# Kernel optimization log

Hardware: AMD Instinct MI355X
Metric: run time of the kernel (lower is better)

The kernel has to match this reference:

```python
import jax, jax.numpy as jnp
import numpy as np

D_MODEL = 1024
D_STATE = 16
D_CONV = 4
EXPAND = 2
D_INNER = EXPAND * D_MODEL          # 2048
DT_RANK = (D_MODEL + 15) // 16      # 64
B_SZ, L = 2, 2048


def setup_inputs() -> dict:
    key = jax.random.key(0)
    ks = jax.random.split(key, 14)
    s = 0.02
    dt_init = jax.random.uniform(ks[10], (D_INNER,), minval=1e-3, maxval=0.1)
    A = jnp.tile(jnp.arange(1, D_STATE + 1, dtype=jnp.float32)[None, :], (D_INNER, 1))
    return {
        "x_f": jax.random.normal(ks[0], (B_SZ, L, D_MODEL), jnp.float32),
        "x_h": jax.random.normal(ks[1], (B_SZ, L, D_MODEL), jnp.float32),
        "W_hf": s * jax.random.normal(ks[2], (D_MODEL, D_MODEL), jnp.float32),
        "b_hf": jnp.zeros((D_MODEL,), jnp.float32),
        "W_in": s * jax.random.normal(ks[3], (2 * D_INNER, D_MODEL), jnp.float32),
        "conv_w": s * jax.random.normal(ks[4], (D_INNER, 1, D_CONV), jnp.float32),
        "conv_b": jnp.zeros((D_INNER,), jnp.float32),
        "W_x": s * jax.random.normal(ks[5], (DT_RANK + 2 * D_STATE, D_INNER), jnp.float32),
        "W_dt": (DT_RANK ** -0.5) * jax.random.normal(ks[6], (D_INNER, DT_RANK), jnp.float32),
        "b_dt": jnp.log(jnp.expm1(dt_init)),
        "A_log": jnp.log(A),
        "D": jnp.ones((D_INNER,), jnp.float32),
        "W_out": s * jax.random.normal(ks[7], (D_MODEL, D_INNER), jnp.float32),
    }


def _mamba(x, W_in, conv_w, conv_b, W_x, W_dt, b_dt, A_log, D, W_out):
    B, Lx, _ = x.shape
    # in_proj -> x, z branches  [B, L, 2*d_inner]
    xz = jnp.einsum("bld,ed->ble", x, W_in)
    x_in, z = jnp.split(xz, 2, axis=-1)
    # causal depthwise conv1d, kernel d_conv, groups = d_inner
    x_nch = jnp.transpose(x_in, (0, 2, 1))  # [B, d_inner, L]
    x_conv = jax.lax.conv_general_dilated(
        x_nch, conv_w, window_strides=(1,), padding=[(D_CONV - 1, 0)],
        dimension_numbers=("NCH", "OIH", "NCH"), feature_group_count=D_INNER)
    x_c = jax.nn.silu(jnp.transpose(x_conv, (0, 2, 1)) + conv_b)  # [B, L, d_inner]
    # input-dependent dt, B, C
    x_dbl = jnp.einsum("ble,fe->blf", x_c, W_x)
    dt_r = x_dbl[..., :DT_RANK]
    B_ssm = x_dbl[..., DT_RANK:DT_RANK + D_STATE]          # [B, L, d_state]
    C_ssm = x_dbl[..., DT_RANK + D_STATE:]                  # [B, L, d_state]
    dt = jax.nn.softplus(jnp.einsum("blr,er->ble", dt_r, W_dt) + b_dt)  # [B, L, d_inner]
    A = -jnp.exp(A_log)  # [d_inner, d_state]

    # selective scan over time; carry h: [B, d_inner, d_state]
    def step(h, inp):
        dt_t, B_t, C_t, x_t = inp  # [B,d_inner], [B,d_state], [B,d_state], [B,d_inner]
        dA = jnp.exp(dt_t[:, :, None] * A)                       # [B, d_inner, d_state]
        dBx = dt_t[:, :, None] * B_t[:, None, :] * x_t[:, :, None]
        h = dA * h + dBx
        y_t = jnp.einsum("bes,bs->be", h, C_t)
        return h, y_t

    seq = (jnp.transpose(dt, (1, 0, 2)), jnp.transpose(B_ssm, (1, 0, 2)),
           jnp.transpose(C_ssm, (1, 0, 2)), jnp.transpose(x_c, (1, 0, 2)))
    h0 = jnp.zeros((B, D_INNER, D_STATE), x.dtype)
    _, ys = jax.lax.scan(step, h0, seq)
    y = jnp.transpose(ys, (1, 0, 2)) + D * x_c   # skip term
    y = y * jax.nn.silu(z)                        # output gate
    return jnp.einsum("ble,de->bld", y, W_out)


def reference(x_f, x_h, W_hf, b_hf, W_in, conv_w, conv_b, W_x, W_dt, b_dt, A_log, D, W_out):
    hf_gate = jax.nn.sigmoid(jnp.einsum("bld,ed->ble", x_h, W_hf) + b_hf)
    modulated = x_f * hf_gate
    return _mamba(modulated, W_in, conv_w, conv_b, W_x, W_dt, b_dt, A_log, D, W_out)
```

## Files before the change

kernel.cpp:

```cpp
#include <hip/hip_runtime.h>
#include <hip/hip_bf16.h>
#include <math.h>

#define L_SEQ  2048
#define BATCH  2
#define DMODEL 1024
#define DINNER 2048
#define DSTATE 16
#define NCHUNK 32
#define LCH    (L_SEQ / NCHUNK)

typedef __attribute__((ext_vector_type(8))) short bf16x8;
typedef __attribute__((ext_vector_type(4))) float f32x4;

__device__ __forceinline__ unsigned short f2bu(float x) {
    __hip_bfloat16 h = __float2bfloat16(x);
    return __builtin_bit_cast(unsigned short, h);
}
__device__ __forceinline__ float fast_exp2(float x) {
    float r; asm("v_exp_f32 %0, %1" : "=v"(r) : "v"(x)); return r;
}
#define LOG2E 1.44269504088896f

__global__ __launch_bounds__(256) void cvt_bf16(
    const float* __restrict__ s, __hip_bfloat16* __restrict__ d)
{
    const int i = (blockIdx.x * 256 + threadIdx.x) * 4;
    const float4 v = *reinterpret_cast<const float4*>(&s[i]);
    ushort4 u;
    u.x = f2bu(v.x); u.y = f2bu(v.y); u.z = f2bu(v.z); u.w = f2bu(v.w);
    *reinterpret_cast<ushort4*>(&d[i]) = u;
}

__global__ __launch_bounds__(256) void cvt_pad_wx(
    const float* __restrict__ s, __hip_bfloat16* __restrict__ d)
{
    const int i = (blockIdx.x * 256 + threadIdx.x) * 4;
    const int r = i >> 11;
    ushort4 u = {0, 0, 0, 0};
    if (r < 96) {
        const float4 v = *reinterpret_cast<const float4*>(&s[i]);
        u.x = f2bu(v.x); u.y = f2bu(v.y); u.z = f2bu(v.z); u.w = f2bu(v.w);
    }
    *reinterpret_cast<ushort4*>(&d[i]) = u;
}

template <int EPI>
__global__ __launch_bounds__(256) void mfma_gemm(
    const __hip_bfloat16* __restrict__ A, int lda,
    const __hip_bfloat16* __restrict__ Bw, int ldb,
    int ksz,
    float* __restrict__ Cf, int ldc,
    __hip_bfloat16* __restrict__ Cb,
    __hip_bfloat16* __restrict__ Cb2,
    const float* __restrict__ bias,
    const float* __restrict__ mul, int ldmul)
{
    __shared__ unsigned short As[2][128 * 32];
    __shared__ unsigned short Bs[2][128 * 32];
    const int tid = threadIdx.x;
    const int row0 = blockIdx.y * 128;
    const int col0 = blockIdx.x * 128;
    const int wid = tid >> 6, lane = tid & 63;
    const int wr = wid >> 1, wc = wid & 1;
    const int fr = lane & 15, fq = lane >> 4;
    const int kz0 = blockIdx.z * ksz;

    f32x4 acc[4][4];
#pragma unroll
    for (int i = 0; i < 4; i++)
#pragma unroll
        for (int j = 0; j < 4; j++) acc[i][j] = (f32x4){0.f, 0.f, 0.f, 0.f};

    const int i0 = tid, i1 = tid + 256;
    const size_t ga0 = (size_t)(row0 + (i0 >> 2)) * lda + (i0 & 3) * 8;
    const size_t ga1 = (size_t)(row0 + (i1 >> 2)) * lda + (i1 & 3) * 8;
    const size_t gb0 = (size_t)(col0 + (i0 >> 2)) * ldb + (i0 & 3) * 8;
    const size_t gb1 = (size_t)(col0 + (i1 >> 2)) * ldb + (i1 & 3) * 8;
    const int nk = ksz >> 5;

#if __has_builtin(__builtin_amdgcn_global_load_lds)
    auto STAGE = [&](int buf, int koff) {
        __builtin_amdgcn_global_load_lds(
            (const __attribute__((address_space(1))) unsigned int*)(A + ga0 + koff),
            (__attribute__((address_space(3))) unsigned int*)&As[buf][i0 * 8], 16, 0, 0);
        __builtin_amdgcn_global_load_lds(
            (const __attribute__((address_space(1))) unsigned int*)(A + ga1 + koff),
            (__attribute__((address_space(3))) unsigned int*)&As[buf][i1 * 8], 16, 0, 0);
        __builtin_amdgcn_global_load_lds(
            (const __attribute__((address_space(1))) unsigned int*)(Bw + gb0 + koff),
            (__attribute__((address_space(3))) unsigned int*)&Bs[buf][i0 * 8], 16, 0, 0);
        __builtin_amdgcn_global_load_lds(
            (const __attribute__((address_space(1))) unsigned int*)(Bw + gb1 + koff),
            (__attribute__((address_space(3))) unsigned int*)&Bs[buf][i1 * 8], 16, 0, 0);
    };
    STAGE(0, kz0);
    __syncthreads();
    for (int kk = 0; kk < nk; kk++) {
        const int cur = kk & 1;
        if (kk + 1 < nk) STAGE(cur ^ 1, kz0 + (kk + 1) * 32);
        bf16x8 af[4], bq[4];
#pragma unroll
        for (int rb = 0; rb < 4; rb++)
            af[rb] = *reinterpret_cast<const bf16x8*>(
                &As[cur][(wr * 64 + rb * 16 + fr) * 32 + fq * 8]);
#pragma unroll
        for (int cb = 0; cb < 4; cb++)
            bq[cb] = *reinterpret_cast<const bf16x8*>(
                &Bs[cur][(wc * 64 + cb * 16 + fr) * 32 + fq * 8]);
#pragma unroll
        for (int rb = 0; rb < 4; rb++)
#pragma unroll
            for (int cb = 0; cb < 4; cb++)
                acc[rb][cb] = __builtin_amdgcn_mfma_f32_16x16x32_bf16(
                    af[rb], bq[cb], acc[rb][cb], 0, 0, 0);
        __syncthreads();
    }
#else
    for (int kk = 0; kk < nk; kk++) {
        const int koff = kz0 + kk * 32;
        const uint4 va0 = *reinterpret_cast<const uint4*>(A + ga0 + koff);
        const uint4 va1 = *reinterpret_cast<const uint4*>(A + ga1 + koff);
        const uint4 vb0 = *reinterpret_cast<const uint4*>(Bw + gb0 + koff);
        const uint4 vb1 = *reinterpret_cast<const uint4*>(Bw + gb1 + koff);
        __syncthreads();
        *reinterpret_cast<uint4*>(&As[0][i0 * 8]) = va0;
        *reinterpret_cast<uint4*>(&As[0][i1 * 8]) = va1;
        *reinterpret_cast<uint4*>(&Bs[0][i0 * 8]) = vb0;
        *reinterpret_cast<uint4*>(&Bs[0][i1 * 8]) = vb1;
        __syncthreads();
        bf16x8 af[4], bq[4];
#pragma unroll
        for (int rb = 0; rb < 4; rb++)
            af[rb] = *reinterpret_cast<const bf16x8*>(
                &As[0][(wr * 64 + rb * 16 + fr) * 32 + fq * 8]);
#pragma unroll
        for (int cb = 0; cb < 4; cb++)
            bq[cb] = *reinterpret_cast<const bf16x8*>(
                &Bs[0][(wc * 64 + cb * 16 + fr) * 32 + fq * 8]);
#pragma unroll
        for (int rb = 0; rb < 4; rb++)
#pragma unroll
            for (int cb = 0; cb < 4; cb++)
                acc[rb][cb] = __builtin_amdgcn_mfma_f32_16x16x32_bf16(
                    af[rb], bq[cb], acc[rb][cb], 0, 0, 0);
    }
#endif

    float* Cz = Cf;
    if (EPI == 0)
        Cz = Cf + (size_t)blockIdx.z * (size_t)(gridDim.y * 128) * ldc;
    const int r0 = row0 + wr * 64, c0 = col0 + wc * 64;
#pragma unroll
    for (int rb = 0; rb < 4; rb++)
#pragma unroll
        for (int cb = 0; cb < 4; cb++) {
            const int col = c0 + cb * 16 + fr;
#pragma unroll
            for (int j = 0; j < 4; j++) {
                const int row = r0 + rb * 16 + fq * 4 + j;
                float v = acc[rb][cb][j];
                if (EPI == 0) {
                    Cz[(size_t)row * ldc + col] = v;
                } else if (EPI == 1) {
                    v = 1.f / (1.f + __expf(-(v + bias[col])));
                    v *= mul[(size_t)row * ldmul + col];
                    Cb[(size_t)row * ldc + col] = __float2bfloat16(v);
                } else if (EPI == 2) {
                    if (col0 < 2048) Cb[(size_t)row * 2048 + col] = __float2bfloat16(v);
                    else             Cb2[(size_t)row * 2048 + col - 2048] = __float2bfloat16(v);
                } else {
                    v += bias[col];
                    v = (v > 20.f) ? v : log1pf(__expf(v));
                    Cf[(size_t)row * ldc + col] = v;
                }
            }
        }
}

__global__ __launch_bounds__(256) void reduce_xdbl(
    const float* __restrict__ part, float* __restrict__ xdbl,
    __hip_bfloat16* __restrict__ dtr)
{
    const int i = blockIdx.x * 256 + threadIdx.x;
    float s = 0.f;
#pragma unroll
    for (int j = 0; j < 4; j++) s += part[(size_t)j * 524288 + i];
    xdbl[i] = s;
    const int col = i & 127;
    if (col < 64) dtr[((i >> 7) << 6) + col] = __float2bfloat16(s);
}

__global__ __launch_bounds__(256) void conv_silu_kernel(
    const __hip_bfloat16* __restrict__ xin_b, const float* __restrict__ cw,
    const float* __restrict__ cb, __hip_bfloat16* __restrict__ xcb)
{
    int gid = blockIdx.x * 256 + threadIdx.x;
    int e = gid & (DINNER - 1);
    int row = gid >> 11;
    int t = row & (L_SEQ - 1);
    float s = cb[e];
#pragma unroll
    for (int j = 0; j < 4; j++) {
        int tt = t - 3 + j;
        if (tt >= 0)
            s = fmaf(cw[e * 4 + j],
                     __bfloat162float(xin_b[(size_t)(row - 3 + j) * 2048 + e]), s);
    }
    xcb[(size_t)row * 2048 + e] = __float2bfloat16(s / (1.f + __expf(-s)));
}

__global__ __launch_bounds__(256) void scan_pass_a(
    const float* __restrict__ dtp, const __hip_bfloat16* __restrict__ xcb,
    const float* __restrict__ xdbl, const float* __restrict__ A_log,
    float* __restrict__ hloc, float* __restrict__ Pp)
{
    __shared__ float sB[LCH][16];
    const int tid = threadIdx.x;
    const int e = (blockIdx.x << 8) + tid;
    const int chunk = blockIdx.y;
    const int b = blockIdx.z;
    const int t0 = chunk * LCH;

    {
        const int r = tid >> 2, sl = tid & 3;
        *(float4*)&sB[r][sl * 4] =
            *(const float4*)&xdbl[(size_t)(b * L_SEQ + t0 + r) * 128 + 64 + sl * 4];
    }
    float av[16];
#pragma unroll
    for (int sq = 0; sq < 4; sq++) {
        const float4 al = *(const float4*)&A_log[e * 16 + sq * 4];
#pragma unroll
        for (int j = 0; j < 4; j++)
            av[sq * 4 + j] = -fast_exp2(((const float*)&al)[j] * LOG2E);
    }
    float h[16];
#pragma unroll
    for (int s = 0; s < 16; s++) h[s] = 0.f;
    float sdt = 0.f;
    __syncthreads();

    const size_t rb = (size_t)(b * L_SEQ + t0) * 2048 + e;
    float dtv_n = dtp[rb];
    float xv_n = __bfloat162float(xcb[rb]);
    for (int t = 0; t < LCH; t++) {
        const float dtv = dtv_n, xv = xv_n;
        if (t + 1 < LCH) {
            dtv_n = dtp[rb + (size_t)(t + 1) * 2048];
            xv_n = __bfloat162float(xcb[rb + (size_t)(t + 1) * 2048]);
        }
        sdt += dtv;
        const float dtx = dtv * xv;
        const float dl2 = dtv * LOG2E;
#pragma unroll
        for (int sq = 0; sq < 4; sq++) {
            const float4 B4 = *(const float4*)&sB[t][sq * 4];
#pragma unroll
            for (int j = 0; j < 4; j++) {
                const int s = sq * 4 + j;
                const float Bv = ((const float*)&B4)[j];
                h[s] = fmaf(fast_exp2(dl2 * av[s]), h[s], Bv * dtx);
            }
        }
    }
    const size_t o = (((size_t)chunk * BATCH + b) * 2048 + e) * 16;
#pragma unroll
    for (int sq = 0; sq < 4; sq++) {
        *(float4*)&hloc[o + sq * 4] =
            make_float4(h[sq * 4], h[sq * 4 + 1], h[sq * 4 + 2], h[sq * 4 + 3]);
        *(float4*)&Pp[o + sq * 4] = make_float4(
            fast_exp2(av[sq * 4] * sdt * LOG2E),
            fast_exp2(av[sq * 4 + 1] * sdt * LOG2E),
            fast_exp2(av[sq * 4 + 2] * sdt * LOG2E),
            fast_exp2(av[sq * 4 + 3] * sdt * LOG2E));
    }
}

__global__ __launch_bounds__(256) void scan_pass_b(
    const float* __restrict__ hloc, const float* __restrict__ Pp,
    float* __restrict__ h0)
{
    const int idx = blockIdx.x * 256 + threadIdx.x;
    float h = 0.f;
    h0[idx] = 0.f;
    for (int c = 0; c < NCHUNK - 1; c++) {
        h = fmaf(Pp[(size_t)c * 65536 + idx], h, hloc[(size_t)c * 65536 + idx]);
        h0[(size_t)(c + 1) * 65536 + idx] = h;
    }
}

__global__ __launch_bounds__(256) void scan_pass_c(
    const float* __restrict__ dtp, const __hip_bfloat16* __restrict__ xcb,
    const float* __restrict__ xdbl, const __hip_bfloat16* __restrict__ zb,
    const float* __restrict__ A_log, const float* __restrict__ Dw,
    const float* __restrict__ h0, __hip_bfloat16* __restrict__ yb)
{
    __shared__ float sB[LCH][16];
    __shared__ float sC[LCH][16];
    const int tid = threadIdx.x;
    const int e = (blockIdx.x << 8) + tid;
    const int chunk = blockIdx.y;
    const int b = blockIdx.z;
    const int t0 = chunk * LCH;

    {
        const int r = tid >> 2, sl = tid & 3;
        const size_t base = (size_t)(b * L_SEQ + t0 + r) * 128;
        *(float4*)&sB[r][sl * 4] = *(const float4*)&xdbl[base + 64 + sl * 4];
        *(float4*)&sC[r][sl * 4] = *(const float4*)&xdbl[base + 80 + sl * 4];
    }
    float av[16];
#pragma unroll
    for (int sq = 0; sq < 4; sq++) {
        const float4 al = *(const float4*)&A_log[e * 16 + sq * 4];
#pragma unroll
        for (int j = 0; j < 4; j++)
            av[sq * 4 + j] = -fast_exp2(((const float*)&al)[j] * LOG2E);
    }
    const float De = Dw[e];
    float h[16];
    const size_t o = (((size_t)chunk * BATCH + b) * 2048 + e) * 16;
#pragma unroll
    for (int sq = 0; sq < 4; sq++) {
        const float4 hv = *(const float4*)&h0[o + sq * 4];
        h[sq * 4] = hv.x; h[sq * 4 + 1] = hv.y;
        h[sq * 4 + 2] = hv.z; h[sq * 4 + 3] = hv.w;
    }
    __syncthreads();

    const size_t rb = (size_t)(b * L_SEQ + t0) * 2048 + e;
    float dtv_n = dtp[rb];
    float xv_n = __bfloat162float(xcb[rb]);
    float zv_n = __bfloat162float(zb[rb]);
    for (int t = 0; t < LCH; t++) {
        const float dtv = dtv_n, xv = xv_n, zv = zv_n;
        if (t + 1 < LCH) {
            dtv_n = dtp[rb + (size_t)(t + 1) * 2048];
            xv_n = __bfloat162float(xcb[rb + (size_t)(t + 1) * 2048]);
            zv_n = __bfloat162float(zb[rb + (size_t)(t + 1) * 2048]);
        }
        const float dtx = dtv * xv;
        const float dl2 = dtv * LOG2E;
        float yp0 = 0.f, yp1 = 0.f, yp2 = 0.f, yp3 = 0.f;
#pragma unroll
        for (int sq = 0; sq < 4; sq++) {
            const float4 B4 = *(const float4*)&sB[t][sq * 4];
            const float4 C4 = *(const float4*)&sC[t][sq * 4];
#pragma unroll
            for (int j = 0; j < 4; j++) {
                const int s = sq * 4 + j;
                const float Bv = ((const float*)&B4)[j];
                const float Cv = ((const float*)&C4)[j];
                h[s] = fmaf(fast_exp2(dl2 * av[s]), h[s], Bv * dtx);
                if (sq == 0) yp0 = fmaf(h[s], Cv, yp0);
                else if (sq == 1) yp1 = fmaf(h[s], Cv, yp1);
                else if (sq == 2) yp2 = fmaf(h[s], Cv, yp2);
                else yp3 = fmaf(h[s], Cv, yp3);
            }
        }
        float yv = (yp0 + yp1) + (yp2 + yp3);
        yv = fmaf(De, xv, yv);
        const float sig = 1.f / (1.f + __expf(-zv));
        yb[rb + (size_t)t * 2048] = __float2bfloat16(yv * zv * sig);
    }
}

extern "C" void kernel_launch(void* const* d_in, const int* in_sizes, int n_in,
                              void* d_out, int out_size, void* d_ws, size_t ws_size,
                              hipStream_t stream)
{
    const float* x_f    = (const float*)d_in[0];
    const float* x_h    = (const float*)d_in[1];
    const float* W_hf   = (const float*)d_in[2];
    const float* b_hf   = (const float*)d_in[3];
    const float* W_in   = (const float*)d_in[4];
    const float* conv_w = (const float*)d_in[5];
    const float* conv_b = (const float*)d_in[6];
    const float* W_x    = (const float*)d_in[7];
    const float* W_dt   = (const float*)d_in[8];
    const float* b_dt   = (const float*)d_in[9];
    const float* A_log  = (const float*)d_in[10];
    const float* Dw     = (const float*)d_in[11];
    const float* W_out  = (const float*)d_in[12];
    float* out = (float*)d_out;
    float* ws  = (float*)d_ws;

    __hip_bfloat16* wout_b = (__hip_bfloat16*)(ws);
    __hip_bfloat16* win_b  = (__hip_bfloat16*)(ws + 1048576);
    __hip_bfloat16* xh_b   = (__hip_bfloat16*)(ws + 3145728);
    __hip_bfloat16* whf_b  = (__hip_bfloat16*)(ws + 5242880);
    __hip_bfloat16* m_b    = (__hip_bfloat16*)(ws + 5767168);
    float*          hloc   = ws + 1048576;
    float*          Pp     = ws + 3145728;
    float*          h0     = ws + 5242880;
    __hip_bfloat16* wx_b   = (__hip_bfloat16*)(ws + 7864320);
    __hip_bfloat16* wdt_b  = (__hip_bfloat16*)(ws + 7995392);
    __hip_bfloat16* dtr_b  = (__hip_bfloat16*)(ws + 8060928);
    float*          part   = ws + 8192000;
    float*          xdbl   = ws + 10289152;
    __hip_bfloat16* xin_b  = (__hip_bfloat16*)(ws + 10813440);
    __hip_bfloat16* z_b    = (__hip_bfloat16*)(ws + 15007744);
    __hip_bfloat16* xc_b   = (__hip_bfloat16*)(ws + 19202048);
    float*          dtp    = ws + 23396352;
    __hip_bfloat16* yb     = (__hip_bfloat16*)(ws + 31784960);

    cvt_bf16<<<2048, 256, 0, stream>>>(W_out, wout_b);
    cvt_bf16<<<4096, 256, 0, stream>>>(W_in,  win_b);
    cvt_bf16<<<4096, 256, 0, stream>>>(x_h,   xh_b);
    cvt_bf16<<<1024, 256, 0, stream>>>(W_hf,  whf_b);
    cvt_pad_wx<<<256, 256, 0, stream>>>(W_x, wx_b);
    cvt_bf16<<<128, 256, 0, stream>>>(W_dt, wdt_b);

    mfma_gemm<1><<<dim3(8, 32, 1), 256, 0, stream>>>(
        xh_b, DMODEL, whf_b, DMODEL, DMODEL,
        nullptr, DMODEL, m_b, nullptr, b_hf, x_f, DMODEL);

    mfma_gemm<2><<<dim3(32, 32, 1), 256, 0, stream>>>(
        m_b, DMODEL, win_b, DMODEL, DMODEL,
        nullptr, 2048, xin_b, z_b, nullptr, nullptr, 0);

    conv_silu_kernel<<<32768, 256, 0, stream>>>(
        xin_b, conv_w, conv_b, xc_b);

    mfma_gemm<0><<<dim3(1, 32, 4), 256, 0, stream>>>(
        xc_b, DINNER, wx_b, DINNER, 512,
        part, 128, nullptr, nullptr, nullptr, nullptr, 0);
    reduce_xdbl<<<2048, 256, 0, stream>>>(part, xdbl, dtr_b);

    mfma_gemm<3><<<dim3(16, 32, 1), 256, 0, stream>>>(
        dtr_b, 64, wdt_b, 64, 64,
        dtp, 2048, nullptr, nullptr, b_dt, nullptr, 0);

    scan_pass_a<<<dim3(8, NCHUNK - 1, BATCH), 256, 0, stream>>>(
        dtp, xc_b, xdbl, A_log, hloc, Pp);
    scan_pass_b<<<256, 256, 0, stream>>>(hloc, Pp, h0);
    scan_pass_c<<<dim3(8, NCHUNK, BATCH), 256, 0, stream>>>(
        dtp, xc_b, xdbl, z_b, A_log, Dw, h0, yb);

    mfma_gemm<0><<<dim3(8, 32, 1), 256, 0, stream>>>(
        yb, DINNER, wout_b, DINNER, DINNER,
        out, DMODEL, nullptr, nullptr, nullptr, nullptr, 0);
}
```

Before: 314.9 us.

## Triple-buffer GEMM LDS staging, merge conversion kernels, widen x_proj split-K

The GEMM main loop moves from double to triple buffering. It prefetches two k-tiles ahead and waits with explicit vmcnt counts instead of a full __syncthreads, so global loads overlap more with MFMA work. The six fp32-to-bf16 conversion launches become one launch that dispatches on block index. The x_proj split-K goes from 4 to 8 slices, with the partial buffer relocated into the dtp region. This adds 50% more LDS per block, which may lower occupancy, and the partial buffer now aliases dtp, which is safe only because dtp is written after the reduction.

```diff
diff --git a/kernel.cpp b/kernel.cpp
--- a/kernel.cpp
+++ b/kernel.cpp
@@ -22,26 +22,37 @@
 }
 #define LOG2E 1.44269504088896f
 
-__global__ __launch_bounds__(256) void cvt_bf16(
-    const float* __restrict__ s, __hip_bfloat16* __restrict__ d)
-{
-    const int i = (blockIdx.x * 256 + threadIdx.x) * 4;
+__global__ __launch_bounds__(256) void cvt_all(
+    const float* __restrict__ Wout, const float* __restrict__ Win,
+    const float* __restrict__ xh,   const float* __restrict__ Whf,
+    const float* __restrict__ Wx,   const float* __restrict__ Wdt,
+    __hip_bfloat16* __restrict__ dWout, __hip_bfloat16* __restrict__ dWin,
+    __hip_bfloat16* __restrict__ dxh,   __hip_bfloat16* __restrict__ dWhf,
+    __hip_bfloat16* __restrict__ dWx,   __hip_bfloat16* __restrict__ dWdt)
+{
+    int bid = blockIdx.x;
+    const float* s; __hip_bfloat16* d;
+    if (bid < 2048)       { s = Wout; d = dWout; }
+    else if (bid < 6144)  { s = Win;  d = dWin;  bid -= 2048; }
+    else if (bid < 10240) { s = xh;   d = dxh;   bid -= 6144; }
+    else if (bid < 11264) { s = Whf;  d = dWhf;  bid -= 10240; }
+    else if (bid < 11520) {
+        bid -= 11264;
+        const int i = (bid * 256 + threadIdx.x) * 4;
+        const int r = i >> 11;
+        ushort4 u = {0, 0, 0, 0};
+        if (r < 96) {
+            const float4 v = *reinterpret_cast<const float4*>(&Wx[i]);
+            u.x = f2bu(v.x); u.y = f2bu(v.y); u.z = f2bu(v.z); u.w = f2bu(v.w);
+        }
+        *reinterpret_cast<ushort4*>(&dWx[i]) = u;
+        return;
+    }
+    else                  { s = Wdt;  d = dWdt;  bid -= 11520; }
+    const int i = (bid * 256 + threadIdx.x) * 4;
     const float4 v = *reinterpret_cast<const float4*>(&s[i]);
     ushort4 u;
     u.x = f2bu(v.x); u.y = f2bu(v.y); u.z = f2bu(v.z); u.w = f2bu(v.w);
-    *reinterpret_cast<ushort4*>(&d[i]) = u;
-}
-
-__global__ __launch_bounds__(256) void cvt_pad_wx(
-    const float* __restrict__ s, __hip_bfloat16* __restrict__ d)
-{
-    const int i = (blockIdx.x * 256 + threadIdx.x) * 4;
-    const int r = i >> 11;
-    ushort4 u = {0, 0, 0, 0};
-    if (r < 96) {
-        const float4 v = *reinterpret_cast<const float4*>(&s[i]);
-        u.x = f2bu(v.x); u.y = f2bu(v.y); u.z = f2bu(v.z); u.w = f2bu(v.w);
-    }
     *reinterpret_cast<ushort4*>(&d[i]) = u;
 }
 
@@ -56,8 +67,8 @@
     const float* __restrict__ bias,
     const float* __restrict__ mul, int ldmul)
 {
-    __shared__ unsigned short As[2][128 * 32];
-    __shared__ unsigned short Bs[2][128 * 32];
+    __shared__ unsigned short As[3][128 * 32];
+    __shared__ unsigned short Bs[3][128 * 32];
     const int tid = threadIdx.x;
     const int row0 = blockIdx.y * 128;
     const int col0 = blockIdx.x * 128;
@@ -95,10 +106,13 @@
             (__attribute__((address_space(3))) unsigned int*)&Bs[buf][i1 * 8], 16, 0, 0);
     };
     STAGE(0, kz0);
-    __syncthreads();
+    STAGE(1, kz0 + 32);
+    asm volatile("s_waitcnt vmcnt(4)" ::: "memory");
+    __builtin_amdgcn_s_barrier();
+    __builtin_amdgcn_sched_barrier(0);
     for (int kk = 0; kk < nk; kk++) {
-        const int cur = kk & 1;
-        if (kk + 1 < nk) STAGE(cur ^ 1, kz0 + (kk + 1) * 32);
+        const int cur = kk % 3;
+        if (kk + 2 < nk) STAGE((kk + 2) % 3, kz0 + (kk + 2) * 32);
         bf16x8 af[4], bq[4];
 #pragma unroll
         for (int rb = 0; rb < 4; rb++)
@@ -114,7 +128,15 @@
             for (int cb = 0; cb < 4; cb++)
                 acc[rb][cb] = __builtin_amdgcn_mfma_f32_16x16x32_bf16(
                     af[rb], bq[cb], acc[rb][cb], 0, 0, 0);
-        __syncthreads();
+        if (kk + 1 < nk) {
+            if (kk + 2 < nk) {
+                asm volatile("s_waitcnt vmcnt(4)" ::: "memory");
+            } else {
+                asm volatile("s_waitcnt vmcnt(0)" ::: "memory");
+            }
+            __builtin_amdgcn_s_barrier();
+            __builtin_amdgcn_sched_barrier(0);
+        }
     }
 #else
     for (int kk = 0; kk < nk; kk++) {
@@ -185,7 +207,7 @@
     const int i = blockIdx.x * 256 + threadIdx.x;
     float s = 0.f;
 #pragma unroll
-    for (int j = 0; j < 4; j++) s += part[(size_t)j * 524288 + i];
+    for (int j = 0; j < 8; j++) s += part[(size_t)j * 524288 + i];
     xdbl[i] = s;
     const int col = i & 127;
     if (col < 64) dtr[((i >> 7) << 6) + col] = __float2bfloat16(s);
@@ -397,20 +419,17 @@
     __hip_bfloat16* wx_b   = (__hip_bfloat16*)(ws + 7864320);
     __hip_bfloat16* wdt_b  = (__hip_bfloat16*)(ws + 7995392);
     __hip_bfloat16* dtr_b  = (__hip_bfloat16*)(ws + 8060928);
-    float*          part   = ws + 8192000;
     float*          xdbl   = ws + 10289152;
     __hip_bfloat16* xin_b  = (__hip_bfloat16*)(ws + 10813440);
     __hip_bfloat16* z_b    = (__hip_bfloat16*)(ws + 15007744);
     __hip_bfloat16* xc_b   = (__hip_bfloat16*)(ws + 19202048);
+    float*          part   = ws + 23396352;
     float*          dtp    = ws + 23396352;
     __hip_bfloat16* yb     = (__hip_bfloat16*)(ws + 31784960);
 
-    cvt_bf16<<<2048, 256, 0, stream>>>(W_out, wout_b);
-    cvt_bf16<<<4096, 256, 0, stream>>>(W_in,  win_b);
-    cvt_bf16<<<4096, 256, 0, stream>>>(x_h,   xh_b);
-    cvt_bf16<<<1024, 256, 0, stream>>>(W_hf,  whf_b);
-    cvt_pad_wx<<<256, 256, 0, stream>>>(W_x, wx_b);
-    cvt_bf16<<<128, 256, 0, stream>>>(W_dt, wdt_b);
+    cvt_all<<<11648, 256, 0, stream>>>(
+        W_out, W_in, x_h, W_hf, W_x, W_dt,
+        wout_b, win_b, xh_b, whf_b, wx_b, wdt_b);
 
     mfma_gemm<1><<<dim3(8, 32, 1), 256, 0, stream>>>(
         xh_b, DMODEL, whf_b, DMODEL, DMODEL,
@@ -423,8 +442,8 @@
     conv_silu_kernel<<<32768, 256, 0, stream>>>(
         xin_b, conv_w, conv_b, xc_b);
 
-    mfma_gemm<0><<<dim3(1, 32, 4), 256, 0, stream>>>(
-        xc_b, DINNER, wx_b, DINNER, 512,
+    mfma_gemm<0><<<dim3(1, 32, 8), 256, 0, stream>>>(
+        xc_b, DINNER, wx_b, DINNER, 256,
         part, 128, nullptr, nullptr, nullptr, nullptr, 0);
     reduce_xdbl<<<2048, 256, 0, stream>>>(part, xdbl, dtr_b);
 
```

New measurement: 313.7 us. No clear change (-0.4%).
